# Kernel optimization log

Hardware: AMD Instinct MI355X
Metric: run time of the kernel (lower is better)

## Reference

```python
import jax, jax.numpy as jnp
import numpy as np

B, T, C = 4, 2048, 2048
N_HEAD = 16
HEAD_DIM = C // N_HEAD
ROPE_BASE = 10000.0


def setup_inputs() -> dict:
    key = jax.random.key(0)
    k1, k2, k3 = jax.random.split(key, 3)
    x = jax.random.normal(k1, (B, T, C), dtype=jnp.float32)
    w_attn = jax.random.normal(k2, (3 * C, C), dtype=jnp.float32) * (1.0 / np.sqrt(C))
    w_proj = jax.random.normal(k3, (C, C), dtype=jnp.float32) * (1.0 / np.sqrt(C))
    return {"x": x, "w_attn": w_attn, "w_proj": w_proj}


def _apply_rope(x, cos, sin):
    # x: [B, H, T, hd]; interleaved pairs (even, odd) rotated
    x_ = x.reshape(*x.shape[:-1], -1, 2)
    x0, x1 = x_[..., 0], x_[..., 1]
    x0r = x0 * cos - x1 * sin
    x1r = x0 * sin + x1 * cos
    return jnp.stack([x0r, x1r], axis=-1).reshape(x.shape)


def reference(x, w_attn, w_proj):
    Bx, Tx, Cx = x.shape
    hd = Cx // N_HEAD
    d = hd // 2

    qkv = jnp.einsum('btc,fc->btf', x, w_attn)  # [B,T,3C]
    q, k, v = jnp.split(qkv, 3, axis=-1)

    def to_heads(t):
        return t.reshape(Bx, Tx, N_HEAD, hd).transpose(0, 2, 1, 3)  # [B,H,T,hd]

    q, k, v = to_heads(q), to_heads(k), to_heads(v)

    # RoPE
    theta = 1.0 / (ROPE_BASE ** (2.0 * jnp.arange(d, dtype=jnp.float32) / hd))
    t = jnp.arange(Tx, dtype=x.dtype)
    freqs = jnp.outer(t, theta.astype(x.dtype))  # [T, d]
    cos = jnp.cos(freqs)[None, None]  # [1,1,T,d]
    sin = jnp.sin(freqs)[None, None]
    q = _apply_rope(q, cos, sin)
    k = _apply_rope(k, cos, sin)

    # Causal attention
    scale = 1.0 / jnp.sqrt(jnp.asarray(hd, dtype=x.dtype))
    scores = jnp.einsum('bhqd,bhkd->bhqk', q, k) * scale
    causal = jnp.tril(jnp.ones((Tx, Tx), dtype=bool))
    scores = jnp.where(causal[None, None], scores, jnp.asarray(-jnp.inf, dtype=scores.dtype))
    attn = jax.nn.softmax(scores, axis=-1)
    y = jnp.einsum('bhqk,bhkd->bhqd', attn, v)  # [B,H,T,hd]

    y = y.transpose(0, 2, 1, 3).reshape(Bx, Tx, Cx)
    return jnp.einsum('btc,oc->bto', y, w_proj)
```

## Files before the change

### kernel.cpp

```cpp
#include <hip/hip_runtime.h>

#define B_ 4
#define T_ 2048
#define C_ 2048
#define H_ 16
#define N1_ 6144
#define M_ 8192
#define SCALE_ 0.08838834764831845f

typedef unsigned short u16;
typedef __bf16 bf16x8 __attribute__((ext_vector_type(8)));
typedef float f32x4 __attribute__((ext_vector_type(4)));
typedef float f32x16 __attribute__((ext_vector_type(16)));

__device__ __forceinline__ u16 f2bf(float f) {
  union { float f; unsigned u; } v; v.f = f;
  return (u16)((v.u + 0x7fffu + ((v.u >> 16) & 1u)) >> 16);
}
__device__ __forceinline__ float bf2f(u16 h) {
  union { unsigned u; float f; } v; v.u = ((unsigned)h) << 16;
  return v.f;
}

__device__ __forceinline__ void gld16(const void* g, void* l) {
  __builtin_amdgcn_global_load_lds(
      (__attribute__((address_space(1))) unsigned int*)(unsigned long long)g,
      (__attribute__((address_space(3))) unsigned int*)(unsigned)(unsigned long long)l,
      16, 0, 0);
}

__global__ void k_cast(const float* __restrict__ in, u16* __restrict__ out, int n4) {
  int i = blockIdx.x * 256 + threadIdx.x;
  if (i >= n4) return;
  float4 v = reinterpret_cast<const float4*>(in)[i];
  ushort4 o;
  o.x = f2bf(v.x); o.y = f2bf(v.y); o.z = f2bf(v.z); o.w = f2bf(v.w);
  reinterpret_cast<ushort4*>(out)[i] = o;
}

__global__ void k_trig(float2* __restrict__ trig) {
  int idx = blockIdx.x * 256 + threadIdx.x;
  int t = idx >> 6, i = idx & 63;
  float theta = __expf(-(float)i * 0.14391156831212787f);
  float f = (float)t * theta;
  float s, c;
  sincosf(f, &s, &c);
  trig[idx] = make_float2(c, s);
}


#define STAGE_H(BUF, AB, HALF, KT, GSH)                                          \
  {                                                                              \
    _Pragma("unroll") for (int q = 0; q < 2; ++q) {                              \
      int c = tid + q * 512;                                                     \
      int idx = c >> 3;                                                          \
      int row = (idx & ((1 << (GSH)) - 1)) + ((HALF) << (GSH)) +                 \
                ((idx >> (GSH)) << ((GSH) + 1));                                 \
      gld16(((AB) ? Bg : Ag) + (long)row * 2048 + (long)(KT) * 64 +              \
                (((c & 7) ^ (idx & 7)) << 3),                                    \
            (char*)&lds[BUF][AB][row * 64 + (c & 7) * 8]);                       \
    }                                                                            \
  }

#define PHASE(BUF, MH, NH, RDA, RDB, STAGE_CODE, WAIT_CODE)                      \
  {                                                                              \
    __builtin_amdgcn_s_barrier();                                                \
    __builtin_amdgcn_sched_barrier(0);                                           \
    if (RDA) {                                                                   \
      _Pragma("unroll") for (int fr = 0; fr < 4; ++fr)                           \
        _Pragma("unroll") for (int ks = 0; ks < 2; ++ks)                         \
          aCur[fr][ks] = *reinterpret_cast<const bf16x8*>(                       \
              &lds[BUF][0][(wm * 128 + (MH) * 64 + fr * 16 + l15) * 64 +         \
                           (((ks * 4 + lq) ^ swl) << 3)]);                       \
    }                                                                            \
    if (RDB) {                                                                   \
      _Pragma("unroll") for (int fc = 0; fc < 2; ++fc)                           \
        _Pragma("unroll") for (int ks = 0; ks < 2; ++ks)                         \
          bKp[NH][fc][ks] = *reinterpret_cast<const bf16x8*>(                    \
              &lds[BUF][1][(wn * 64 + (NH) * 32 + fc * 16 + l15) * 64 +          \
                           (((ks * 4 + lq) ^ swl) << 3)]);                       \
    }                                                                            \
    STAGE_CODE;                                                                  \
    __builtin_amdgcn_s_setprio(1);                                               \
    _Pragma("unroll") for (int fr = 0; fr < 4; ++fr)                             \
      _Pragma("unroll") for (int fc = 0; fc < 2; ++fc)                           \
        _Pragma("unroll") for (int ks = 0; ks < 2; ++ks)                         \
          acc[(MH) * 4 + fr][(NH) * 2 + fc] =                                    \
              __builtin_amdgcn_mfma_f32_16x16x32_bf16(                           \
                  aCur[fr][ks], bKp[NH][fc][ks],                                 \
                  acc[(MH) * 4 + fr][(NH) * 2 + fc], 0, 0, 0);                   \
    __builtin_amdgcn_s_setprio(0);                                               \
    WAIT_CODE;                                                                   \
  }

template <int EPI>
__global__ __launch_bounds__(512, 2) void k_gemm8(
    const u16* __restrict__ A, const u16* __restrict__ Bt,
    float* __restrict__ Cf,
    u16* __restrict__ qh, u16* __restrict__ kh, u16* __restrict__ vt,
    const float2* __restrict__ trig, int nbx, int cpx) {
  __shared__ alignas(16) u16 lds[2][2][256 * 64];
  const int tid = threadIdx.x;
  const int lane = tid & 63;
  const int w = tid >> 6;
  const int wm = w >> 2;
  const int wn = w & 3;
  const int l15 = lane & 15, lq = lane >> 4;
  const int swl = l15 & 7;

  const int id = (int)blockIdx.x;
  const int swz = (id & 7) * cpx + (id >> 3);
  const int bx = swz % nbx, by = swz / nbx;
  const long rowBase = (long)by * 256;
  const long colBase = (long)bx * 256;
  const u16* Ag = A + rowBase * 2048;
  const u16* Bg = Bt + colBase * 2048;

  const f32x4 z4 = {0.f, 0.f, 0.f, 0.f};
  f32x4 acc[8][4];
#pragma unroll
  for (int m = 0; m < 8; ++m)
#pragma unroll
    for (int n = 0; n < 4; ++n) acc[m][n] = z4;
  bf16x8 aCur[4][2], bKp[2][2][2];

  STAGE_H(0, 0, 0, 0, 6); STAGE_H(0, 1, 0, 0, 5);
  STAGE_H(0, 0, 1, 0, 6); STAGE_H(0, 1, 1, 0, 5);
  STAGE_H(1, 0, 0, 1, 6); STAGE_H(1, 1, 0, 1, 5);
  asm volatile("s_waitcnt vmcnt(4)" ::: "memory");

#pragma unroll 1
  for (int i = 0; i < 16; ++i) {
    const int t1 = 2 * i + 1, t2 = 2 * i + 2, t3 = 2 * i + 3;
    const bool st = (i < 15);
    PHASE(0, 0, 0, 1, 1, STAGE_H(1, 0, 1, t1, 6), );
    PHASE(0, 0, 1, 0, 1, STAGE_H(1, 1, 1, t1, 5), );
    PHASE(0, 1, 0, 1, 0, if (st) STAGE_H(0, 0, 0, t2, 6), );
    PHASE(0, 1, 1, 0, 0, if (st) STAGE_H(0, 1, 0, t2, 5),
          if (st) { asm volatile("s_waitcnt vmcnt(4)" ::: "memory"); }
          else    { asm volatile("s_waitcnt vmcnt(0)" ::: "memory"); });
    PHASE(1, 0, 0, 1, 1, if (st) STAGE_H(0, 0, 1, t2, 6), );
    PHASE(1, 0, 1, 0, 1, if (st) STAGE_H(0, 1, 1, t2, 5), );
    PHASE(1, 1, 0, 1, 0, if (st) STAGE_H(1, 0, 0, t3, 6), );
    PHASE(1, 1, 1, 0, 0, if (st) STAGE_H(1, 1, 0, t3, 5),
          if (st) { asm volatile("s_waitcnt vmcnt(4)" ::: "memory"); });
  }

  if (EPI == 0) {
#pragma unroll
    for (int fr = 0; fr < 8; ++fr) {
      long row0 = rowBase + wm * 128 + fr * 16 + lq * 4;
#pragma unroll
      for (int fc = 0; fc < 4; ++fc) {
        long col = colBase + wn * 64 + fc * 16 + l15;
#pragma unroll
        for (int j = 0; j < 4; ++j)
          Cf[(row0 + j) * 2048 + col] = acc[fr][fc][j];
      }
    }
  } else {
    const int sec = (int)(colBase >> 11);
#pragma unroll
    for (int fr = 0; fr < 8; ++fr) {
      int row0 = (int)rowBase + wm * 128 + fr * 16 + lq * 4;
      int b = row0 >> 11;
      int t0 = row0 & (T_ - 1);
#pragma unroll
      for (int fc = 0; fc < 4; ++fc) {
        int cc = (int)colBase + wn * 64 + fc * 16;
        int hh = (cc >> 7) & 15;
        int dd = (cc & 127) + l15;
        long bh = (long)b * H_ + hh;
        if (sec < 2) {
          u16* dst = sec ? kh : qh;
#pragma unroll
          for (int j = 0; j < 4; ++j) {
            float v = acc[fr][fc][j];
            float vp = __shfl_xor(v, 1);
            float2 cs = trig[(t0 + j) * 64 + (dd >> 1)];
            float r = (dd & 1) ? (vp * cs.y + v * cs.x) : (v * cs.x - vp * cs.y);
            dst[(bh * T_ + t0 + j) * 128 + dd] = f2bf(r);
          }
        } else {
          ushort4 pk;
          pk.x = f2bf(acc[fr][fc][0]); pk.y = f2bf(acc[fr][fc][1]);
          pk.z = f2bf(acc[fr][fc][2]); pk.w = f2bf(acc[fr][fc][3]);
          *reinterpret_cast<ushort4*>(&vt[(bh * 128 + dd) * T_ + t0]) = pk;
        }
      }
    }
  }
}

#define PACK_SLOT(dst, P, base)                                                       \
  {                                                                                   \
    unsigned ua, ub, uc, ud;                                                          \
    asm("v_cvt_pk_bf16_f32 %0, %1, %2" : "=v"(ua) : "v"(P[base + 0]), "v"(P[base + 1])); \
    asm("v_cvt_pk_bf16_f32 %0, %1, %2" : "=v"(ub) : "v"(P[base + 4]), "v"(P[base + 5])); \
    asm("v_permlane32_swap_b32 %0, %1" : "+v"(ua), "+v"(ub));                         \
    asm("v_cvt_pk_bf16_f32 %0, %1, %2" : "=v"(uc) : "v"(P[base + 2]), "v"(P[base + 3])); \
    asm("v_cvt_pk_bf16_f32 %0, %1, %2" : "=v"(ud) : "v"(P[base + 6]), "v"(P[base + 7])); \
    asm("v_permlane32_swap_b32 %0, %1" : "+v"(uc), "+v"(ud));                         \
    union { unsigned u[4]; bf16x8 v; } tt;                                            \
    tt.u[0] = ua; tt.u[1] = uc; tt.u[2] = ub; tt.u[3] = ud;                           \
    dst = tt.v;                                                                       \
  }

__global__ __launch_bounds__(256, 2) void k_attn(
    const u16* __restrict__ qh, const u16* __restrict__ kh,
    const u16* __restrict__ vt, u16* __restrict__ ym) {
  __shared__ alignas(16) u16 lK[2][64 * 128];
  __shared__ alignas(16) u16 lV[2][128 * 64];
  const int tid = threadIdx.x;
  const int lane = tid & 63;
  const int w = tid >> 6;
  const int l31 = lane & 31;
  const int hi = lane >> 5;
  const int swz = (l31 & 7) << 4;
  const int id = (int)blockIdx.x;
  const int pr = id >> 6;
  const int bh = ((id & 7) << 3) | ((id >> 3) & 7);
  const int b = bh >> 4, hh = bh & 15;
  const u16* Kbase = kh + (long)bh * T_ * 128;
  const u16* Vbase = vt + (long)bh * 128 * T_;
  const u16* Qbase = qh + (long)bh * T_ * 128;

  auto stage = [&](int bi, int t0) {
#pragma unroll
    for (int i = 0; i < 4; ++i) {
      int c = tid + i * 256;
      int rK = c >> 4;
      int lbK = ((c & 15) << 4) ^ ((rK & 7) << 4);
      gld16(Kbase + (long)(t0 + rK) * 128 + (lbK >> 1), (char*)(&lK[bi][0]) + c * 16);
      int dV = c >> 3;
      int lbV = ((c & 7) << 4) ^ ((dV & 7) << 4);
      gld16(Vbase + (long)dV * T_ + t0 + (lbV >> 1), (char*)(&lV[bi][0]) + c * 16);
    }
  };

#pragma unroll 1
  for (int half = 0; half < 2; ++half) {
    const int p = half ? 15 - pr : pr;
    const int NT = 2 * (p + 1);
    const int qw = p * 128 + w * 32;
    const int ntw = (qw + 95) >> 6;

    bf16x8 qF[8];
    {
      const u16* qrow = Qbase + (long)(qw + l31) * 128 + hi * 8;
#pragma unroll
      for (int s = 0; s < 8; ++s)
        qF[s] = *reinterpret_cast<const bf16x8*>(qrow + s * 16);
    }

    f32x16 oA[4];
#pragma unroll
    for (int n = 0; n < 4; ++n)
#pragma unroll
      for (int r = 0; r < 16; ++r) oA[n][r] = 0.f;
    float mR = -1e30f, lR = 0.f;

    stage(0, 0);
    __syncthreads();
    int cur = 0;
#pragma unroll 1
    for (int jt = 0; jt < NT; ++jt) {
      if (jt + 1 < NT) stage(cur ^ 1, (jt + 1) * 64);
      if (jt < ntw) {
        const int t0 = jt * 64;
        const char* Kc = (const char*)(&lK[cur][0]);
        const char* Vc = (const char*)(&lV[cur][0]);
        f32x16 s0, s1;
#pragma unroll
        for (int r = 0; r < 16; ++r) { s0[r] = 0.f; s1[r] = 0.f; }
        __builtin_amdgcn_s_setprio(1);
#pragma unroll
        for (int s = 0; s < 8; ++s) {
          int cb = (s * 32 + hi * 16) ^ swz;
          bf16x8 k0 = *reinterpret_cast<const bf16x8*>(Kc + l31 * 256 + cb);
          bf16x8 k1 = *reinterpret_cast<const bf16x8*>(Kc + (32 + l31) * 256 + cb);
          s0 = __builtin_amdgcn_mfma_f32_32x32x16_bf16(k0, qF[s], s0, 0, 0, 0);
          s1 = __builtin_amdgcn_mfma_f32_32x32x16_bf16(k1, qF[s], s1, 0, 0, 0);
        }
        __builtin_amdgcn_s_setprio(0);

        float f0[16], f1[16];
#pragma unroll
        for (int r = 0; r < 16; ++r) { f0[r] = s0[r] * SCALE_; f1[r] = s1[r] * SCALE_; }
        if (jt == ntw - 1) {
          const int qa = qw + l31;
#pragma unroll
          for (int r = 0; r < 16; ++r) {
            int kv = t0 + (r & 3) + 8 * (r >> 2) + 4 * hi;
            if (kv > qa) f0[r] = -1e30f;
            if (kv + 32 > qa) f1[r] = -1e30f;
          }
        }
        float mt = fmaxf(f0[0], f1[0]);
#pragma unroll
        for (int r = 1; r < 16; ++r) mt = fmaxf(mt, fmaxf(f0[r], f1[r]));
        mt = fmaxf(mt, __shfl_xor(mt, 32));
        float mN = fmaxf(mR, mt);
        float al = __expf(mR - mN);
        mR = mN;
        float rs = 0.f;
#pragma unroll
        for (int r = 0; r < 16; ++r) {
          f0[r] = __expf(f0[r] - mN);
          f1[r] = __expf(f1[r] - mN);
          rs += f0[r] + f1[r];
        }
        rs += __shfl_xor(rs, 32);
        lR = lR * al + rs;
        float aR[16];
#pragma unroll
        for (int r = 0; r < 16; ++r)
          aR[r] = __shfl(al, (r & 3) + 8 * (r >> 2) + 4 * hi);
#pragma unroll
        for (int n = 0; n < 4; ++n)
#pragma unroll
          for (int r = 0; r < 16; ++r) oA[n][r] *= aR[r];

        bf16x8 paF[4];
        PACK_SLOT(paF[0], f0, 0);
        PACK_SLOT(paF[1], f0, 8);
        PACK_SLOT(paF[2], f1, 0);
        PACK_SLOT(paF[3], f1, 8);

        __builtin_amdgcn_s_setprio(1);
#pragma unroll
        for (int n = 0; n < 4; ++n) {
          const char* vrow = Vc + (n * 32 + l31) * 128;
#pragma unroll
          for (int ks = 0; ks < 4; ++ks) {
            bf16x8 bV = *reinterpret_cast<const bf16x8*>(vrow + ((ks * 32 + hi * 16) ^ swz));
            oA[n] = __builtin_amdgcn_mfma_f32_32x32x16_bf16(paF[ks], bV, oA[n], 0, 0, 0);
          }
        }
        __builtin_amdgcn_s_setprio(0);
      }
      __syncthreads();
      cur ^= 1;
    }

    float li = 1.f / lR;
    float liR[16];
#pragma unroll
    for (int r = 0; r < 16; ++r)
      liR[r] = __shfl(li, (r & 3) + 8 * (r >> 2) + 4 * hi);
    u16* yrow = ym + ((long)b * T_ + qw) * C_ + hh * 128 + l31;
#pragma unroll
    for (int n = 0; n < 4; ++n)
#pragma unroll
      for (int r = 0; r < 16; ++r) {
        int cr = (r & 3) + 8 * (r >> 2) + 4 * hi;
        yrow[(long)cr * C_ + n * 32] = f2bf(oA[n][r] * liR[r]);
      }
  }
}

extern "C" void kernel_launch(void* const* d_in, const int* in_sizes, int n_in,
                              void* d_out, int out_size, void* d_ws, size_t ws_size,
                              hipStream_t stream) {
  (void)in_sizes; (void)n_in; (void)out_size; (void)ws_size;
  const float* x = (const float*)d_in[0];
  const float* wa = (const float*)d_in[1];
  const float* wp = (const float*)d_in[2];
  float* out = (float*)d_out;
  char* ws = (char*)d_ws;

  size_t off = 0;
  auto alloc = [&](size_t bytes) -> char* {
    char* p = ws + off;
    off += (bytes + 255) & ~(size_t)255;
    return p;
  };
  u16* xb  = (u16*)alloc((size_t)M_ * C_ * 2);
  u16* wab = (u16*)alloc((size_t)N1_ * C_ * 2);
  u16* wpb = (u16*)alloc((size_t)C_ * C_ * 2);
  u16* qh  = (u16*)alloc((size_t)64 * T_ * 128 * 2);
  u16* kh  = (u16*)alloc((size_t)64 * T_ * 128 * 2);
  u16* vt  = (u16*)alloc((size_t)64 * 128 * T_ * 2);
  float2* trig = (float2*)alloc((size_t)T_ * 64 * 8);
  u16* ym = xb;

  k_cast<<<dim3((M_ * C_ / 4) / 256), 256, 0, stream>>>(x, xb, M_ * C_ / 4);
  k_cast<<<dim3((N1_ * C_ / 4) / 256), 256, 0, stream>>>(wa, wab, N1_ * C_ / 4);
  k_cast<<<dim3((C_ * C_ / 4) / 256), 256, 0, stream>>>(wp, wpb, C_ * C_ / 4);
  k_trig<<<dim3((T_ * 64) / 256), 256, 0, stream>>>(trig);
  k_gemm8<1><<<dim3(768), 512, 0, stream>>>(
      xb, wab, nullptr, qh, kh, vt, trig, 24, 96);
  k_attn<<<dim3(512), 256, 0, stream>>>(qh, kh, vt, ym);
  k_gemm8<0><<<dim3(256), 512, 0, stream>>>(
      ym, wpb, out, nullptr, nullptr, nullptr, nullptr, 8, 32);
}
```

Measured before the change: 408.4 us.

## Double-buffer GEMM register fragments and reschedule LDS reads against MFMA

Restructures the GEMM main loop so A and B fragments are ping-ponged between two register sets, with the next fragment's LDS reads issued while the current MFMA quadrant runs. It also reorders and regroups the global-to-LDS half-tile stages and retunes the vmcnt waits and barriers, prefetching the full second k-tile in the prologue. The intent is to hide LDS read latency and shorten the exposed barrier waits between phases. In exchange it uses more VGPRs under the 512x2 launch bound, which risks spills, and the hand-placed wait counts make correctness depend on the exact order of the issued loads.

```diff
diff --git a/kernel.cpp b/kernel.cpp
--- a/kernel.cpp
+++ b/kernel.cpp
@@ -62,36 +62,40 @@
     }                                                                            \
   }
 
-#define PHASE(BUF, MH, NH, RDA, RDB, STAGE_CODE, WAIT_CODE)                      \
+#define RD_A(DST, BUF, MH)                                                       \
   {                                                                              \
-    __builtin_amdgcn_s_barrier();                                                \
-    __builtin_amdgcn_sched_barrier(0);                                           \
-    if (RDA) {                                                                   \
-      _Pragma("unroll") for (int fr = 0; fr < 4; ++fr)                           \
-        _Pragma("unroll") for (int ks = 0; ks < 2; ++ks)                         \
-          aCur[fr][ks] = *reinterpret_cast<const bf16x8*>(                       \
-              &lds[BUF][0][(wm * 128 + (MH) * 64 + fr * 16 + l15) * 64 +         \
-                           (((ks * 4 + lq) ^ swl) << 3)]);                       \
-    }                                                                            \
-    if (RDB) {                                                                   \
-      _Pragma("unroll") for (int fc = 0; fc < 2; ++fc)                           \
-        _Pragma("unroll") for (int ks = 0; ks < 2; ++ks)                         \
-          bKp[NH][fc][ks] = *reinterpret_cast<const bf16x8*>(                    \
-              &lds[BUF][1][(wn * 64 + (NH) * 32 + fc * 16 + l15) * 64 +          \
-                           (((ks * 4 + lq) ^ swl) << 3)]);                       \
-    }                                                                            \
-    STAGE_CODE;                                                                  \
+    _Pragma("unroll") for (int fr = 0; fr < 4; ++fr)                             \
+      _Pragma("unroll") for (int ks = 0; ks < 2; ++ks)                           \
+        DST[fr][ks] = *reinterpret_cast<const bf16x8*>(                          \
+            &lds[BUF][0][(wm * 128 + (MH) * 64 + fr * 16 + l15) * 64 +           \
+                         (((ks * 4 + lq) ^ swl) << 3)]);                         \
+  }
+
+#define RD_B(DST, BUF, NH)                                                       \
+  {                                                                              \
+    _Pragma("unroll") for (int fc = 0; fc < 2; ++fc)                             \
+      _Pragma("unroll") for (int ks = 0; ks < 2; ++ks)                           \
+        DST[fc][ks] = *reinterpret_cast<const bf16x8*>(                          \
+            &lds[BUF][1][(wn * 64 + (NH) * 32 + fc * 16 + l15) * 64 +            \
+                         (((ks * 4 + lq) ^ swl) << 3)]);                         \
+  }
+
+#define MM(QM, QN, AR, BR)                                                       \
+  {                                                                              \
     __builtin_amdgcn_s_setprio(1);                                               \
     _Pragma("unroll") for (int fr = 0; fr < 4; ++fr)                             \
       _Pragma("unroll") for (int fc = 0; fc < 2; ++fc)                           \
         _Pragma("unroll") for (int ks = 0; ks < 2; ++ks)                         \
-          acc[(MH) * 4 + fr][(NH) * 2 + fc] =                                    \
+          acc[(QM) * 4 + fr][(QN) * 2 + fc] =                                    \
               __builtin_amdgcn_mfma_f32_16x16x32_bf16(                           \
-                  aCur[fr][ks], bKp[NH][fc][ks],                                 \
-                  acc[(MH) * 4 + fr][(NH) * 2 + fc], 0, 0, 0);                   \
+                  AR[fr][ks], BR[fc][ks],                                        \
+                  acc[(QM) * 4 + fr][(QN) * 2 + fc], 0, 0, 0);                   \
     __builtin_amdgcn_s_setprio(0);                                               \
-    WAIT_CODE;                                                                   \
-  }
+  }
+
+#define VMW(N) asm volatile("s_waitcnt vmcnt(" #N ")" ::: "memory")
+#define BAR __builtin_amdgcn_s_barrier()
+#define SB0 __builtin_amdgcn_sched_barrier(0)
 
 template <int EPI>
 __global__ __launch_bounds__(512, 2) void k_gemm8(
@@ -122,28 +126,60 @@
   for (int m = 0; m < 8; ++m)
 #pragma unroll
     for (int n = 0; n < 4; ++n) acc[m][n] = z4;
-  bf16x8 aCur[4][2], bKp[2][2][2];
+  bf16x8 aF0[4][2], aF1[4][2], bF0[2][2], bF1[2][2];
 
   STAGE_H(0, 0, 0, 0, 6); STAGE_H(0, 1, 0, 0, 5);
-  STAGE_H(0, 0, 1, 0, 6); STAGE_H(0, 1, 1, 0, 5);
+  STAGE_H(0, 1, 1, 0, 5); STAGE_H(0, 0, 1, 0, 6);
   STAGE_H(1, 0, 0, 1, 6); STAGE_H(1, 1, 0, 1, 5);
-  asm volatile("s_waitcnt vmcnt(4)" ::: "memory");
+  STAGE_H(1, 1, 1, 1, 5); STAGE_H(1, 0, 1, 1, 6);
+  VMW(8);
+  BAR; SB0;
+  RD_A(aF0, 0, 0); RD_B(bF0, 0, 0);
+  SB0;
 
 #pragma unroll 1
   for (int i = 0; i < 16; ++i) {
-    const int t1 = 2 * i + 1, t2 = 2 * i + 2, t3 = 2 * i + 3;
+    const int t2 = 2 * i + 2, t3 = 2 * i + 3;
     const bool st = (i < 15);
-    PHASE(0, 0, 0, 1, 1, STAGE_H(1, 0, 1, t1, 6), );
-    PHASE(0, 0, 1, 0, 1, STAGE_H(1, 1, 1, t1, 5), );
-    PHASE(0, 1, 0, 1, 0, if (st) STAGE_H(0, 0, 0, t2, 6), );
-    PHASE(0, 1, 1, 0, 0, if (st) STAGE_H(0, 1, 0, t2, 5),
-          if (st) { asm volatile("s_waitcnt vmcnt(4)" ::: "memory"); }
-          else    { asm volatile("s_waitcnt vmcnt(0)" ::: "memory"); });
-    PHASE(1, 0, 0, 1, 1, if (st) STAGE_H(0, 0, 1, t2, 6), );
-    PHASE(1, 0, 1, 0, 1, if (st) STAGE_H(0, 1, 1, t2, 5), );
-    PHASE(1, 1, 0, 1, 0, if (st) STAGE_H(1, 0, 0, t3, 6), );
-    PHASE(1, 1, 1, 0, 0, if (st) STAGE_H(1, 1, 0, t3, 5),
-          if (st) { asm volatile("s_waitcnt vmcnt(4)" ::: "memory"); });
+    BAR; SB0;
+    RD_B(bF1, 0, 1);
+    MM(0, 0, aF0, bF0);
+    VMW(8);
+    BAR; SB0;
+    if (st) STAGE_H(0, 0, 0, t2, 6);
+    MM(0, 1, aF0, bF1);
+    RD_A(aF1, 0, 1);
+    SB0;
+    BAR; SB0;
+    if (st) STAGE_H(0, 1, 0, t2, 5);
+    MM(1, 0, aF1, bF0);
+    if (st) { VMW(8); } else { VMW(4); }
+    BAR; SB0;
+    RD_B(bF0, 1, 0);
+    if (st) { STAGE_H(0, 1, 1, t2, 5); STAGE_H(0, 0, 1, t2, 6); }
+    MM(1, 1, aF1, bF1);
+    if (st) { VMW(10); } else { VMW(2); }
+    RD_A(aF0, 1, 0);
+    SB0;
+    BAR; SB0;
+    RD_B(bF1, 1, 1);
+    MM(0, 0, aF0, bF0);
+    if (st) { VMW(8); } else { VMW(0); }
+    BAR; SB0;
+    if (st) STAGE_H(1, 0, 0, t3, 6);
+    MM(0, 1, aF0, bF1);
+    RD_A(aF1, 1, 1);
+    SB0;
+    BAR; SB0;
+    if (st) { STAGE_H(1, 1, 0, t3, 5); STAGE_H(1, 1, 1, t3, 5); }
+    MM(1, 0, aF1, bF0);
+    if (st) VMW(10);
+    BAR; SB0;
+    if (st) RD_B(bF0, 0, 0);
+    if (st) STAGE_H(1, 0, 1, t3, 6);
+    MM(1, 1, aF1, bF1);
+    if (st) { VMW(10); RD_A(aF0, 0, 0); }
+    SB0;
   }
 
   if (EPI == 0) {
```

After: 624.2 us. 1.53x slower.

## Make QKV GEMM persistent with cross-tile prefetch of next tile's operands

Applied to the files above, without the earlier changes.

The QKV projection GEMM now launches 256 persistent workgroups, each looping over three 256x256 output tiles mapped so that tiles stay within one XCD. The next tile's first K-slices are staged into LDS while the current tile finishes, which hides the pipeline fill and the tail of each tile. The aim is to remove per-workgroup prologue and epilogue bubbles and the scheduling overhead of 768 separate blocks. In exchange, the epilogue stores run while next-tile loads are in flight. The vmcnt waits are retuned for this, and getting those counts wrong could let data be read before it has landed.

```diff
diff --git a/kernel.cpp b/kernel.cpp
--- a/kernel.cpp
+++ b/kernel.cpp
@@ -51,13 +51,14 @@
 
 #define STAGE_H(BUF, AB, HALF, KT, GSH)                                          \
   {                                                                              \
+    const u16* _p = ((KT) < 32) ? ((AB) ? BgC : AgC) : ((AB) ? BgN : AgN);       \
+    const long _kt = (KT) & 31;                                                  \
     _Pragma("unroll") for (int q = 0; q < 2; ++q) {                              \
       int c = tid + q * 512;                                                     \
       int idx = c >> 3;                                                          \
       int row = (idx & ((1 << (GSH)) - 1)) + ((HALF) << (GSH)) +                 \
                 ((idx >> (GSH)) << ((GSH) + 1));                                 \
-      gld16(((AB) ? Bg : Ag) + (long)row * 2048 + (long)(KT) * 64 +              \
-                (((c & 7) ^ (idx & 7)) << 3),                                    \
+      gld16(_p + (long)row * 2048 + _kt * 64 + (((c & 7) ^ (idx & 7)) << 3),     \
             (char*)&lds[BUF][AB][row * 64 + (c & 7) * 8]);                       \
     }                                                                            \
   }
@@ -93,12 +94,16 @@
     WAIT_CODE;                                                                   \
   }
 
+#define VMW(N) asm volatile("s_waitcnt vmcnt(" #N ")" ::: "memory")
+#define BAR __builtin_amdgcn_s_barrier()
+#define SB0 __builtin_amdgcn_sched_barrier(0)
+
 template <int EPI>
 __global__ __launch_bounds__(512, 2) void k_gemm8(
     const u16* __restrict__ A, const u16* __restrict__ Bt,
     float* __restrict__ Cf,
     u16* __restrict__ qh, u16* __restrict__ kh, u16* __restrict__ vt,
-    const float2* __restrict__ trig, int nbx, int cpx) {
+    const float2* __restrict__ trig, int nbx, int ntiles) {
   __shared__ alignas(16) u16 lds[2][2][256 * 64];
   const int tid = threadIdx.x;
   const int lane = tid & 63;
@@ -109,86 +114,98 @@
   const int swl = l15 & 7;
 
   const int id = (int)blockIdx.x;
-  const int swz = (id & 7) * cpx + (id >> 3);
-  const int bx = swz % nbx, by = swz / nbx;
-  const long rowBase = (long)by * 256;
-  const long colBase = (long)bx * 256;
-  const u16* Ag = A + rowBase * 2048;
-  const u16* Bg = Bt + colBase * 2048;
+  const int xcd = id & 7, lid = id >> 3;
 
   const f32x4 z4 = {0.f, 0.f, 0.f, 0.f};
   f32x4 acc[8][4];
-#pragma unroll
-  for (int m = 0; m < 8; ++m)
-#pragma unroll
-    for (int n = 0; n < 4; ++n) acc[m][n] = z4;
   bf16x8 aCur[4][2], bKp[2][2][2];
 
-  STAGE_H(0, 0, 0, 0, 6); STAGE_H(0, 1, 0, 0, 5);
-  STAGE_H(0, 0, 1, 0, 6); STAGE_H(0, 1, 1, 0, 5);
-  STAGE_H(1, 0, 0, 1, 6); STAGE_H(1, 1, 0, 1, 5);
-  asm volatile("s_waitcnt vmcnt(4)" ::: "memory");
-
 #pragma unroll 1
-  for (int i = 0; i < 16; ++i) {
-    const int t1 = 2 * i + 1, t2 = 2 * i + 2, t3 = 2 * i + 3;
-    const bool st = (i < 15);
-    PHASE(0, 0, 0, 1, 1, STAGE_H(1, 0, 1, t1, 6), );
-    PHASE(0, 0, 1, 0, 1, STAGE_H(1, 1, 1, t1, 5), );
-    PHASE(0, 1, 0, 1, 0, if (st) STAGE_H(0, 0, 0, t2, 6), );
-    PHASE(0, 1, 1, 0, 0, if (st) STAGE_H(0, 1, 0, t2, 5),
-          if (st) { asm volatile("s_waitcnt vmcnt(4)" ::: "memory"); }
-          else    { asm volatile("s_waitcnt vmcnt(0)" ::: "memory"); });
-    PHASE(1, 0, 0, 1, 1, if (st) STAGE_H(0, 0, 1, t2, 6), );
-    PHASE(1, 0, 1, 0, 1, if (st) STAGE_H(0, 1, 1, t2, 5), );
-    PHASE(1, 1, 0, 1, 0, if (st) STAGE_H(1, 0, 0, t3, 6), );
-    PHASE(1, 1, 1, 0, 0, if (st) STAGE_H(1, 1, 0, t3, 5),
-          if (st) { asm volatile("s_waitcnt vmcnt(4)" ::: "memory"); });
-  }
-
-  if (EPI == 0) {
-#pragma unroll
-    for (int fr = 0; fr < 8; ++fr) {
-      long row0 = rowBase + wm * 128 + fr * 16 + lq * 4;
-#pragma unroll
-      for (int fc = 0; fc < 4; ++fc) {
-        long col = colBase + wn * 64 + fc * 16 + l15;
-#pragma unroll
-        for (int j = 0; j < 4; ++j)
-          Cf[(row0 + j) * 2048 + col] = acc[fr][fc][j];
+  for (int tj = 0; tj < ntiles; ++tj) {
+    const int tl = xcd * (32 * ntiles) + tj * 32 + lid;
+    const int bx = tl % nbx, by = tl / nbx;
+    const long rowBase = (long)by * 256;
+    const long colBase = (long)bx * 256;
+    const u16* AgC = A + rowBase * 2048;
+    const u16* BgC = Bt + colBase * 2048;
+    const int tjn = (tj + 1 < ntiles) ? tj + 1 : tj;
+    const int tln = xcd * (32 * ntiles) + tjn * 32 + lid;
+    const u16* AgN = A + (long)(tln / nbx) * 256 * 2048;
+    const u16* BgN = Bt + (long)(tln % nbx) * 256 * 2048;
+
+#pragma unroll
+    for (int m = 0; m < 8; ++m)
+#pragma unroll
+      for (int n = 0; n < 4; ++n) acc[m][n] = z4;
+
+    if (tj == 0) {
+      STAGE_H(0, 0, 0, 0, 6); STAGE_H(0, 1, 0, 0, 5);
+      STAGE_H(0, 0, 1, 0, 6); STAGE_H(0, 1, 1, 0, 5);
+      STAGE_H(1, 0, 0, 1, 6); STAGE_H(1, 1, 0, 1, 5);
+      VMW(6);
+    }
+
+#pragma unroll 1
+    for (int i = 0; i < 16; ++i) {
+      const int t1 = 2 * i + 1, t2 = 2 * i + 2, t3 = 2 * i + 3;
+      const bool st = (i < 15) || (tj + 1 < ntiles);
+      PHASE(0, 0, 0, 1, 1, STAGE_H(1, 0, 1, t1, 6), );
+      PHASE(0, 0, 1, 0, 1, STAGE_H(1, 1, 1, t1, 5), );
+      PHASE(0, 1, 0, 1, 0, if (st) STAGE_H(0, 0, 0, t2, 6), );
+      PHASE(0, 1, 1, 0, 0, if (st) STAGE_H(0, 1, 0, t2, 5),
+            if (st) { VMW(4); } else { VMW(0); });
+      PHASE(1, 0, 0, 1, 1, if (st) STAGE_H(0, 0, 1, t2, 6), );
+      PHASE(1, 0, 1, 0, 1, if (st) STAGE_H(0, 1, 1, t2, 5), );
+      PHASE(1, 1, 0, 1, 0, if (st) STAGE_H(1, 0, 0, t3, 6), );
+      PHASE(1, 1, 1, 0, 0, if (st) STAGE_H(1, 1, 0, t3, 5),
+            if (st) { VMW(6); });
+    }
+
+    if (EPI == 0) {
+#pragma unroll
+      for (int fr = 0; fr < 8; ++fr) {
+        long row0 = rowBase + wm * 128 + fr * 16 + lq * 4;
+#pragma unroll
+        for (int fc = 0; fc < 4; ++fc) {
+          long col = colBase + wn * 64 + fc * 16 + l15;
+#pragma unroll
+          for (int j = 0; j < 4; ++j)
+            Cf[(row0 + j) * 2048 + col] = acc[fr][fc][j];
+        }
       }
-    }
-  } else {
-    const int sec = (int)(colBase >> 11);
-#pragma unroll
-    for (int fr = 0; fr < 8; ++fr) {
-      int row0 = (int)rowBase + wm * 128 + fr * 16 + lq * 4;
-      int b = row0 >> 11;
-      int t0 = row0 & (T_ - 1);
-#pragma unroll
-      for (int fc = 0; fc < 4; ++fc) {
-        int cc = (int)colBase + wn * 64 + fc * 16;
-        int hh = (cc >> 7) & 15;
-        int dd = (cc & 127) + l15;
-        long bh = (long)b * H_ + hh;
-        if (sec < 2) {
-          u16* dst = sec ? kh : qh;
-#pragma unroll
-          for (int j = 0; j < 4; ++j) {
-            float v = acc[fr][fc][j];
-            float vp = __shfl_xor(v, 1);
-            float2 cs = trig[(t0 + j) * 64 + (dd >> 1)];
-            float r = (dd & 1) ? (vp * cs.y + v * cs.x) : (v * cs.x - vp * cs.y);
-            dst[(bh * T_ + t0 + j) * 128 + dd] = f2bf(r);
+    } else {
+      const int sec = (int)(colBase >> 11);
+#pragma unroll
+      for (int fr = 0; fr < 8; ++fr) {
+        int row0 = (int)rowBase + wm * 128 + fr * 16 + lq * 4;
+        int b = row0 >> 11;
+        int t0 = row0 & (T_ - 1);
+#pragma unroll
+        for (int fc = 0; fc < 4; ++fc) {
+          int cc = (int)colBase + wn * 64 + fc * 16;
+          int hh = (cc >> 7) & 15;
+          int dd = (cc & 127) + l15;
+          long bh = (long)b * H_ + hh;
+          if (sec < 2) {
+            u16* dst = sec ? kh : qh;
+#pragma unroll
+            for (int j = 0; j < 4; ++j) {
+              float v = acc[fr][fc][j];
+              float vp = __shfl_xor(v, 1);
+              float2 cs = trig[(t0 + j) * 64 + (dd >> 1)];
+              float r = (dd & 1) ? (vp * cs.y + v * cs.x) : (v * cs.x - vp * cs.y);
+              dst[(bh * T_ + t0 + j) * 128 + dd] = f2bf(r);
+            }
+          } else {
+            ushort4 pk;
+            pk.x = f2bf(acc[fr][fc][0]); pk.y = f2bf(acc[fr][fc][1]);
+            pk.z = f2bf(acc[fr][fc][2]); pk.w = f2bf(acc[fr][fc][3]);
+            *reinterpret_cast<ushort4*>(&vt[(bh * 128 + dd) * T_ + t0]) = pk;
           }
-        } else {
-          ushort4 pk;
-          pk.x = f2bf(acc[fr][fc][0]); pk.y = f2bf(acc[fr][fc][1]);
-          pk.z = f2bf(acc[fr][fc][2]); pk.w = f2bf(acc[fr][fc][3]);
-          *reinterpret_cast<ushort4*>(&vt[(bh * 128 + dd) * T_ + t0]) = pk;
         }
       }
     }
+    if (tj + 1 < ntiles) VMW(0);
   }
 }
 
@@ -388,9 +405,9 @@
   k_cast<<<dim3((N1_ * C_ / 4) / 256), 256, 0, stream>>>(wa, wab, N1_ * C_ / 4);
   k_cast<<<dim3((C_ * C_ / 4) / 256), 256, 0, stream>>>(wp, wpb, C_ * C_ / 4);
   k_trig<<<dim3((T_ * 64) / 256), 256, 0, stream>>>(trig);
-  k_gemm8<1><<<dim3(768), 512, 0, stream>>>(
-      xb, wab, nullptr, qh, kh, vt, trig, 24, 96);
+  k_gemm8<1><<<dim3(256), 512, 0, stream>>>(
+      xb, wab, nullptr, qh, kh, vt, trig, 24, 3);
   k_attn<<<dim3(512), 256, 0, stream>>>(qh, kh, vt, ym);
   k_gemm8<0><<<dim3(256), 512, 0, stream>>>(
-      ym, wpb, out, nullptr, nullptr, nullptr, nullptr, 8, 32);
-}
+      ym, wpb, out, nullptr, nullptr, nullptr, nullptr, 8, 1);
+}
```

Result: slower. 426.1 us (+4.3%).
